# Kernel optimization log

Measured on AMD Instinct MI355X. Metric: run time of the kernel, lower is better.

Reference implementation:

```python
import jax, jax.numpy as jnp
import numpy as np

NEIGHBOUR = 3  # matches init_kwargs['neighbour']


def _conv2d(x, w, b=None, stride=1, pad=0):
    out = jax.lax.conv_general_dilated(
        x, w, (stride, stride), [(pad, pad), (pad, pad)],
        dimension_numbers=('NCHW', 'OIHW', 'NCHW'))
    if b is not None:
        out = out + b[None, :, None, None]
    return out


def _warp(x, offset, wg_w, wg_b, conv_w):
    """Deformable bilinear warp: offsets -> 4 corner gathers -> modulate -> regroup -> strided conv."""
    k = NEIGHBOUR
    N = k * k
    B, C, H, W = x.shape
    m = jax.nn.sigmoid(_conv2d(x, wg_w, wg_b, 1, 1))          # [B,N,H,W] modulation gate
    xp = jnp.pad(x, ((0, 0), (0, 0), (1, 1), (1, 1)))         # zero pad -> [B,C,H+2,W+2]
    Hp, Wp = H + 2, W + 2
    r = jnp.arange(-(k - 1) // 2, (k - 1) // 2 + 1, dtype=x.dtype)
    pnx, pny = jnp.meshgrid(r, r, indexing='ij')              # kernel-neighbour offsets p_n
    # absolute sampling positions in padded coords (p_0 starts at 1 due to padding)
    p0x = jnp.arange(1, H + 1, dtype=x.dtype)[None, :, None, None]
    p0y = jnp.arange(1, W + 1, dtype=x.dtype)[None, None, :, None]
    off = offset.transpose(0, 2, 3, 1)                        # [B,H,W,2N]; first N = x, last N = y
    px = p0x + pnx.ravel()[None, None, None, :] + off[..., :N]  # [B,H,W,N]
    py = p0y + pny.ravel()[None, None, None, :] + off[..., N:]
    fx = jnp.floor(jax.lax.stop_gradient(px))                 # p.detach().floor()
    fy = jnp.floor(jax.lax.stop_gradient(py))
    qx_lt = jnp.clip(fx, 0, Hp - 1)
    qy_lt = jnp.clip(fy, 0, Wp - 1)
    qx_rb = jnp.clip(fx + 1, 0, Hp - 1)
    qy_rb = jnp.clip(fy + 1, 0, Wp - 1)
    px = jnp.clip(px, 0, Hp - 1)
    py = jnp.clip(py, 0, Wp - 1)
    # bilinear weights (same algebra as the torch code)
    g_lt = (1 + (qx_lt - px)) * (1 + (qy_lt - py))
    g_rb = (1 - (qx_rb - px)) * (1 - (qy_rb - py))
    g_lb = (1 + (qx_lt - px)) * (1 - (qy_rb - py))
    g_rt = (1 - (qx_rb - px)) * (1 + (qy_lt - py))
    ix_lt = qx_lt.astype(jnp.int32); iy_lt = qy_lt.astype(jnp.int32)
    ix_rb = qx_rb.astype(jnp.int32); iy_rb = qy_rb.astype(jnp.int32)
    x_flat = xp.reshape(B, C, Hp * Wp)

    def gather(ix, iy):
        idx = (ix * Wp + iy).reshape(B, 1, H * W * N)
        return jnp.take_along_axis(x_flat, idx, axis=-1).reshape(B, C, H, W, N)

    xw = (g_lt[:, None] * gather(ix_lt, iy_lt)
          + g_rb[:, None] * gather(ix_rb, iy_rb)
          + g_lb[:, None] * gather(ix_lt, iy_rb)
          + g_rt[:, None] * gather(ix_rb, iy_lt))              # [B,C,H,W,N]
    xw = xw * m.transpose(0, 2, 3, 1)[:, None]                 # modulation, broadcast over C
    # regroup [B,C,H,W,k,k] -> [B,C,H*k,W*k] (matches _reshape_x_warped ordering)
    xw = xw.reshape(B, C, H, W, k, k).transpose(0, 1, 2, 4, 3, 5).reshape(B, C, H * k, W * k)
    return _conv2d(xw, conv_w, None, stride=k, pad=0)          # grouped-back strided conv


def setup_inputs() -> dict:
    B, C, MH, H, W = 4, 64, 18, 128, 128  # MH = 2*neighbour^2
    key = jax.random.key(0)
    ks = jax.random.split(key, 12)
    f32 = jnp.float32
    s = 0.05  # weight scale to keep gates unsaturated
    return {
        'x_t': jax.random.normal(ks[0], (B, C, H, W), f32),
        'pre_offset': jax.random.normal(ks[1], (B, MH, H, W), f32),
        'mean': jax.random.normal(ks[2], (B, MH, H, W), f32),
        'upd_w': s * jax.random.normal(ks[3], (MH, C + MH, 3, 3), f32),
        'upd_b': s * jax.random.normal(ks[4], (MH,), f32),
        'rst_w': s * jax.random.normal(ks[5], (MH, C + MH, 3, 3), f32),
        'rst_b': s * jax.random.normal(ks[6], (MH,), f32),
        'out_w': s * jax.random.normal(ks[7], (MH, C + MH, 3, 3), f32),
        'out_b': s * jax.random.normal(ks[8], (MH,), f32),
        'wg_w': s * jax.random.normal(ks[9], (9, C, 3, 3), f32),
        'wg_b': s * jax.random.normal(ks[10], (9,), f32),
        'warp_conv_w': s * jax.random.normal(ks[11], (C, C, 3, 3), f32),
    }


def reference(x_t, pre_offset, mean, upd_w, upd_b, rst_w, rst_b, out_w, out_b,
              wg_w, wg_b, warp_conv_w):
    stacked = jnp.concatenate([x_t, pre_offset], axis=1)
    update_gate = jax.nn.sigmoid(_conv2d(stacked, upd_w, upd_b, 1, 1))
    reset_gate = jax.nn.sigmoid(_conv2d(stacked, rst_w, rst_b, 1, 1))
    cand = jnp.tanh(_conv2d(jnp.concatenate([x_t, pre_offset * reset_gate], axis=1), out_w, out_b, 1, 1))
    offset = pre_offset * (1 - update_gate) + cand * update_gate
    mean_new = mean + 0.5 * (pre_offset - mean)
    offset = offset + mean_new
    x_out = _warp(x_t, offset, wg_w, wg_b, warp_conv_w)
    return (x_out, offset, mean_new)
```

## Files before the change

kernel.cpp:

```cpp
#include <hip/hip_runtime.h>
#include <hip/hip_bf16.h>
#include <math.h>

#define Bn  4
#define Cc  64
#define MHc 18
#define Hh  128
#define Wd  128
#define HW  (Hh*Wd)
#define Np  9
#define HP  130
#define WP  130
#define XPE (HP*WP*Cc)
#define PPE (HP*WP*32)
#define KX  576
#define KP  288
#define KT  (KX+KP)

typedef __attribute__((ext_vector_type(8))) short short8;
typedef __attribute__((ext_vector_type(4))) float float4v;

__device__ __forceinline__ float bf2f(__hip_bfloat16 x) { return __bfloat162float(x); }
__device__ __forceinline__ __hip_bfloat16 f2bf(float x) { return __float2bfloat16(x); }
__device__ __forceinline__ float sigm(float x) { return 1.f / (1.f + expf(-x)); }

#define NW1 (64*KT)
#define NW2 (32*KP)
#define NW3 (Cc*Cc*Np)

__global__ __launch_bounds__(256)
void k_prep(const float* __restrict__ x, const float* __restrict__ po,
            const float* __restrict__ upd_w, const float* __restrict__ rst_w,
            const float* __restrict__ out_w, const float* __restrict__ wg_w,
            const float* __restrict__ wcw,
            __hip_bfloat16* __restrict__ xp, __hip_bfloat16* __restrict__ pp,
            __hip_bfloat16* __restrict__ wall, __hip_bfloat16* __restrict__ w2,
            __hip_bfloat16* __restrict__ wt) {
  __shared__ float tile[16][65];
  int blk = blockIdx.x;
  int t = threadIdx.x;
  if (blk < 4096) {
    int wtile = blk & 7;
    int h = (blk >> 3) & 127;
    int b = blk >> 10;
    int w0 = wtile * 16;
    int wa = t & 15, cq = t >> 4;
    #pragma unroll
    for (int j = 0; j < 4; ++j) {
      int c = cq * 4 + j;
      tile[wa][c] = x[(b*Cc + c)*HW + h*Wd + w0 + wa];
    }
    __syncthreads();
    int cb = t & 63, wq = t >> 6;
    #pragma unroll
    for (int j = 0; j < 4; ++j) {
      int w = wq * 4 + j;
      xp[b*XPE + ((h+1)*WP + (w0 + w + 1))*Cc + cb] = f2bf(tile[w][cb]);
    }
  } else if (blk < 4608) {
    int pb = blk - 4096;
    int h = pb & 127;
    int b = pb >> 7;
    int w = t & 127;
    int half = t >> 7;
    for (int j = 0; j < 9; ++j) {
      int ch = half * 9 + j;
      float v = po[(b*MHc + ch)*HW + h*Wd + w];
      pp[b*PPE + ((h+1)*WP + (w+1))*32 + ch] = f2bf(v);
    }
  } else {
    int idx = (blk - 4608) * 256 + t;
    if (idx < NW1) {
      int k  = idx % KT;
      int gr = idx / KT;
      float v = 0.f;
      if (k < KX) {
        int n = k >> 6, ci = k & 63;
        if      (gr < 18) v = upd_w[(gr*(Cc+MHc) + ci)*9 + n];
        else if (gr < 36) v = rst_w[((gr-18)*(Cc+MHc) + ci)*9 + n];
        else if (gr < 54) v = out_w[((gr-36)*(Cc+MHc) + ci)*9 + n];
        else if (gr < 63) v = wg_w[((gr-54)*Cc + ci)*9 + n];
      } else {
        int kk = k - KX;
        int n = kk >> 5, jc = kk & 31;
        if (jc < 18) {
          if      (gr < 18) v = upd_w[(gr*(Cc+MHc) + Cc + jc)*9 + n];
          else if (gr < 36) v = rst_w[((gr-18)*(Cc+MHc) + Cc + jc)*9 + n];
        }
      }
      wall[idx] = f2bf(v);
    } else if (idx < NW1 + NW2) {
      int i2 = idx - NW1;
      int k  = i2 % KP;
      int oc = i2 / KP;
      int n = k >> 5, jc = k & 31;
      float v = (oc < 18 && jc < 18) ? out_w[(oc*(Cc+MHc) + Cc + jc)*9 + n] : 0.f;
      w2[i2] = f2bf(v);
    } else if (idx < NW1 + NW2 + NW3) {
      int i3 = idx - NW1 - NW2;
      int k  = i3 % 576;
      int co = i3 / 576;
      wt[i3] = f2bf(wcw[(co*Cc + (k & 63))*9 + (k >> 6)]);
    }
  }
}

__global__ __launch_bounds__(256)
void k_gates(const __hip_bfloat16* __restrict__ xpad,
             const __hip_bfloat16* __restrict__ popad,
             const __hip_bfloat16* __restrict__ wall,
             const float* __restrict__ po,
             const float* __restrict__ upd_b,
             const float* __restrict__ rst_b,
             const float* __restrict__ out_b,
             const float* __restrict__ wg_b,
             float* __restrict__ u_out,
             float* __restrict__ cx_out,
             __hip_bfloat16* __restrict__ ropad,
             __hip_bfloat16* __restrict__ m_t) {
  __shared__ __align__(16) __hip_bfloat16 sh[16][KT + 8];
  __shared__ __align__(16) __hip_bfloat16 roL[16][32];
  int blk = blockIdx.x;
  int wtile = blk & 7;
  int h = (blk >> 3) & 127;
  int b = blk >> 10;
  int w0 = wtile * 16;
  int lane = threadIdx.x & 63;
  int wave = threadIdx.x >> 6;
  int t = threadIdx.x;

  ((unsigned int*)roL)[t] = 0u;

  const __hip_bfloat16* xpb = xpad + b * XPE;
  const __hip_bfloat16* ppb = popad + b * PPE;
  int c32 = lane & 31, tsel = lane >> 5;

  for (int tt = 0; tt < 4; ++tt) {
    int pl = wave * 4 + tt;
    int wp = w0 + pl;
    #pragma unroll
    for (int n = 0; n < 9; ++n)
      sh[pl][n*64 + lane] = xpb[((h + n/3)*WP + wp + n%3)*Cc + lane];
    #pragma unroll
    for (int nb = 0; nb < 9; nb += 2) {
      int n = nb + tsel;
      if (n < 9)
        sh[pl][KX + n*32 + c32] = ppb[((h + n/3)*WP + wp + n%3)*32 + c32];
    }
  }
  __syncthreads();

  int mrow = lane & 15;
  int quad = lane >> 4;
  int cotile = wave * 16;
  float4v acc = {0.f, 0.f, 0.f, 0.f};
  for (int ks = 0; ks < KT/32; ++ks) {
    short8 a = *reinterpret_cast<const short8*>(
        wall + (cotile + mrow) * KT + ks * 32 + quad * 8);
    short8 bfr = *reinterpret_cast<const short8*>(
        &sh[mrow][ks * 32 + quad * 8]);
    acc = __builtin_amdgcn_mfma_f32_16x16x32_bf16(a, bfr, acc, 0, 0, 0);
  }

  int sp = h * Wd + w0 + mrow;
  #pragma unroll
  for (int r = 0; r < 4; ++r) {
    int gr = cotile + quad * 4 + r;
    float v = acc[r];
    if (gr < 18) {
      u_out[(b*MHc + gr)*HW + sp] = sigm(v + upd_b[gr]);
    } else if (gr < 36) {
      int oc = gr - 18;
      float rr = sigm(v + rst_b[oc]);
      roL[mrow][oc] = f2bf(rr * po[(b*MHc + oc)*HW + sp]);
    } else if (gr < 54) {
      int oc = gr - 36;
      cx_out[(b*MHc + oc)*HW + sp] = v + out_b[oc];
    } else if (gr < 63) {
      int nn = gr - 54;
      m_t[(b*HW + sp)*9 + nn] = f2bf(sigm(v + wg_b[nn]));
    }
  }
  __syncthreads();
  unsigned int* dst = (unsigned int*)(ropad + b*PPE + ((h+1)*WP + (w0+1))*32);
  dst[t] = ((unsigned int*)roL)[t];
}

__global__ __launch_bounds__(256)
void k_fuse(const __hip_bfloat16* __restrict__ xpad,
            const __hip_bfloat16* __restrict__ ropad,
            const __hip_bfloat16* __restrict__ w2,
            const __hip_bfloat16* __restrict__ wt,
            const __hip_bfloat16* __restrict__ m_t,
            const float* __restrict__ po,
            const float* __restrict__ mean,
            float* __restrict__ out_off,
            float* __restrict__ out_mn,
            float* __restrict__ out_x) {
  __shared__ __align__(16) char lbuf[16*584*2];
  __shared__ float offL[16][18];
  __shared__ float mL[16][9];
  __shared__ __align__(16) float gw[144][4];
  __shared__ __align__(16) int   ga[144][4];
  auto shro = (__hip_bfloat16(*)[KP+8])lbuf;
  auto xw   = (__hip_bfloat16(*)[584])lbuf;

  int blk = blockIdx.x;
  int wtile = blk & 7;
  int h = (blk >> 3) & 127;
  int b = blk >> 10;
  int w0 = wtile * 16;
  int lane = threadIdx.x & 63;
  int wave = threadIdx.x >> 6;
  int t = threadIdx.x;

  const __hip_bfloat16* rpb = ropad + b * PPE;
  int c32 = lane & 31, tsel = lane >> 5;
  for (int tt = 0; tt < 4; ++tt) {
    int pl = wave * 4 + tt;
    int wp = w0 + pl;
    #pragma unroll
    for (int nb = 0; nb < 9; nb += 2) {
      int n = nb + tsel;
      if (n < 9)
        shro[pl][n*32 + c32] = rpb[((h + n/3)*WP + wp + n%3)*32 + c32];
    }
  }
  __syncthreads();

  int mrow = lane & 15;
  int quad = lane >> 4;

  if (wave < 2) {
    float4v acc = {0.f, 0.f, 0.f, 0.f};
    for (int ks = 0; ks < KP/32; ++ks) {
      short8 a = *reinterpret_cast<const short8*>(
          w2 + (wave*16 + mrow) * KP + ks * 32 + quad * 8);
      short8 bfr = *reinterpret_cast<const short8*>(
          &shro[mrow][ks * 32 + quad * 8]);
      acc = __builtin_amdgcn_mfma_f32_16x16x32_bf16(a, bfr, acc, 0, 0, 0);
    }
    int sp = h * Wd + w0 + mrow;
    #pragma unroll
    for (int r = 0; r < 4; ++r) {
      int gr = wave*16 + quad * 4 + r;
      if (gr < 18) {
        int gi = (b*MHc + gr)*HW + sp;
        float cand = tanhf(out_off[gi] + acc[r]);
        float u = out_mn[gi];
        float p = po[gi];
        float mn = 0.5f * (mean[gi] + p);
        float off = p * (1.f - u) + cand * u + mn;
        out_off[gi] = off;
        out_mn[gi]  = mn;
        offL[mrow][gr] = off;
      }
    }
  } else {
    int base = (wave - 2) * 64 + lane;
    #pragma unroll
    for (int rep = 0; rep < 2; ++rep) {
      int id = base + rep * 128;
      if (id < 144) {
        int px = id / 9, n = id % 9;
        mL[px][n] = bf2f(m_t[(b*HW + h*Wd + w0 + px)*9 + n]);
      }
    }
  }
  __syncthreads();

  if (t < 144) {
    int px = t / 9, n = t % 9;
    int wp = w0 + px;
    float ox = offL[px][n];
    float oy = offL[px][9 + n];
    float mn = mL[px][n];
    float px_ = (float)(h + 1) + (float)(n / 3 - 1) + ox;
    float py_ = (float)(wp + 1) + (float)(n % 3 - 1) + oy;
    float fx = floorf(px_), fy = floorf(py_);
    float xlt = fminf(fmaxf(fx,       0.f), 129.f);
    float ylt = fminf(fmaxf(fy,       0.f), 129.f);
    float xrb = fminf(fmaxf(fx + 1.f, 0.f), 129.f);
    float yrb = fminf(fmaxf(fy + 1.f, 0.f), 129.f);
    float pxc = fminf(fmaxf(px_, 0.f), 129.f);
    float pyc = fminf(fmaxf(py_, 0.f), 129.f);
    float glt = (1.f + xlt - pxc) * (1.f + ylt - pyc);
    float grb = (1.f - xrb + pxc) * (1.f - yrb + pyc);
    float glb = (1.f + xlt - pxc) * (1.f - yrb + pyc);
    float grt = (1.f - xrb + pxc) * (1.f + ylt - pyc);
    int ixl = (int)xlt, iyl = (int)ylt, ixr = (int)xrb, iyr = (int)yrb;
    gw[t][0] = glt * mn; gw[t][1] = grb * mn;
    gw[t][2] = glb * mn; gw[t][3] = grt * mn;
    ga[t][0] = (ixl * WP + iyl) * Cc; ga[t][1] = (ixr * WP + iyr) * Cc;
    ga[t][2] = (ixl * WP + iyr) * Cc; ga[t][3] = (ixr * WP + iyl) * Cc;
  }
  __syncthreads();

  const __hip_bfloat16* xpb = xpad + b * XPE;
  for (int tt = 0; tt < 4; ++tt) {
    int pl = wave * 4 + tt;
    #pragma unroll
    for (int n = 0; n < Np; ++n) {
      int q = pl * 9 + n;
      float4v g = *reinterpret_cast<const float4v*>(gw[q]);
      int a0 = ga[q][0], a1 = ga[q][1], a2 = ga[q][2], a3 = ga[q][3];
      float v0 = bf2f(xpb[a0 + lane]);
      float v1 = bf2f(xpb[a1 + lane]);
      float v2 = bf2f(xpb[a2 + lane]);
      float v3 = bf2f(xpb[a3 + lane]);
      xw[pl][n * 64 + lane] = f2bf(g.x*v0 + g.y*v1 + g.z*v2 + g.w*v3);
    }
  }
  __syncthreads();

  int cotile = wave * 16;
  float4v acc = {0.f, 0.f, 0.f, 0.f};
  for (int ks = 0; ks < 18; ++ks) {
    short8 a = *reinterpret_cast<const short8*>(
        wt + (cotile + mrow) * 576 + ks * 32 + quad * 8);
    short8 bfr = *reinterpret_cast<const short8*>(
        &xw[mrow][ks * 32 + quad * 8]);
    acc = __builtin_amdgcn_mfma_f32_16x16x32_bf16(a, bfr, acc, 0, 0, 0);
  }
  #pragma unroll
  for (int r = 0; r < 4; ++r) {
    int co = cotile + quad * 4 + r;
    out_x[((b * Cc + co) * Hh + h) * Wd + w0 + mrow] = acc[r];
  }
}

__global__ void f_convAB(const float* __restrict__ x, const float* __restrict__ po,
                         const float* __restrict__ wA, const float* __restrict__ bA,
                         const float* __restrict__ wB, const float* __restrict__ bB,
                         float* __restrict__ u_scr, float* __restrict__ ro_scr) {
  int idx = blockIdx.x * 256 + threadIdx.x;
  if (idx >= Bn * MHc * HW) return;
  int w = idx & 127, h = (idx >> 7) & 127, oc = (idx >> 14) % MHc, b = idx / (MHc*HW);
  float accA = bA[oc], accB = bB[oc];
  const float* xb = x + b*Cc*HW; const float* pb = po + b*MHc*HW;
  for (int ic = 0; ic < Cc + MHc; ++ic) {
    const float* src = (ic < Cc) ? (xb + ic*HW) : (pb + (ic-Cc)*HW);
    const float* wa = wA + (oc*(Cc+MHc)+ic)*9; const float* wb = wB + (oc*(Cc+MHc)+ic)*9;
    for (int kh = 0; kh < 3; ++kh) { int hh = h+kh-1; if ((unsigned)hh >= Hh) continue;
      for (int kw = 0; kw < 3; ++kw) { int ww = w+kw-1; if ((unsigned)ww >= Wd) continue;
        float v = src[hh*Wd+ww]; accA += v*wa[kh*3+kw]; accB += v*wb[kh*3+kw]; } }
  }
  u_scr[idx] = sigm(accA); ro_scr[idx] = sigm(accB) * pb[oc*HW + h*Wd + w];
}
__global__ void f_convC(const float* __restrict__ x, const float* __restrict__ po,
                        const float* __restrict__ mean, const float* __restrict__ wC,
                        const float* __restrict__ bC, const float* __restrict__ u_scr,
                        const float* __restrict__ ro_scr, float* __restrict__ out_off,
                        float* __restrict__ out_mean) {
  int idx = blockIdx.x * 256 + threadIdx.x;
  if (idx >= Bn * MHc * HW) return;
  int w = idx & 127, h = (idx >> 7) & 127, oc = (idx >> 14) % MHc, b = idx / (MHc*HW);
  float acc = bC[oc];
  const float* xb = x + b*Cc*HW; const float* rb = ro_scr + b*MHc*HW;
  for (int ic = 0; ic < Cc + MHc; ++ic) {
    const float* src = (ic < Cc) ? (xb + ic*HW) : (rb + (ic-Cc)*HW);
    const float* wv = wC + (oc*(Cc+MHc)+ic)*9;
    for (int kh = 0; kh < 3; ++kh) { int hh = h+kh-1; if ((unsigned)hh >= Hh) continue;
      for (int kw = 0; kw < 3; ++kw) { int ww = w+kw-1; if ((unsigned)ww >= Wd) continue;
        acc += src[hh*Wd+ww]*wv[kh*3+kw]; } }
  }
  float cand = tanhf(acc); float u = u_scr[idx]; float p = po[idx];
  float mn = 0.5f*(mean[idx]+p);
  out_off[idx] = p*(1.f-u)+cand*u+mn; out_mean[idx] = mn;
}
__global__ __launch_bounds__(256)
void f_warp(const float* __restrict__ x, const float* __restrict__ off_f,
            const float* __restrict__ wg, const float* __restrict__ bg,
            const float* __restrict__ wc, float* __restrict__ out) {
  __shared__ float mred[4][Np][64]; __shared__ float mval[4][Np];
  __shared__ float xwv[4][Np][64];
  int lane = threadIdx.x & 63, wave = threadIdx.x >> 6;
  int p = blockIdx.x * 4 + wave;
  int b = p >> 14, rem = p & 16383, h = rem >> 7, w = rem & 127;
  const float* xc = x + (b*Cc + lane)*HW;
  float part[Np];
  for (int n = 0; n < Np; ++n) part[n] = 0.f;
  for (int kh = 0; kh < 3; ++kh) { int hh = h+kh-1; if ((unsigned)hh >= Hh) continue;
    for (int kw = 0; kw < 3; ++kw) { int ww = w+kw-1; if ((unsigned)ww >= Wd) continue;
      float v = xc[hh*Wd+ww];
      for (int n = 0; n < Np; ++n) part[n] += v*wg[(n*Cc+lane)*9+kh*3+kw]; } }
  for (int n = 0; n < Np; ++n) mred[wave][n][lane] = part[n];
  __syncthreads();
  if (lane < Np) { float s = bg[lane];
    for (int c = 0; c < Cc; ++c) s += mred[wave][lane][c];
    mval[wave][lane] = sigm(s); }
  __syncthreads();
  const float* offb = off_f + b*MHc*HW; int sp = h*Wd + w;
  for (int n = 0; n < Np; ++n) {
    float px = (float)(h+1) + (float)(n/3-1) + offb[n*HW+sp];
    float py = (float)(w+1) + (float)(n%3-1) + offb[(9+n)*HW+sp];
    float fxq = floorf(px), fyq = floorf(py);
    float xlt = fminf(fmaxf(fxq,0.f),129.f), ylt = fminf(fmaxf(fyq,0.f),129.f);
    float xrb = fminf(fmaxf(fxq+1.f,0.f),129.f), yrb = fminf(fmaxf(fyq+1.f,0.f),129.f);
    float pxc = fminf(fmaxf(px,0.f),129.f), pyc = fminf(fmaxf(py,0.f),129.f);
    float glt = (1.f+xlt-pxc)*(1.f+ylt-pyc), grb = (1.f-xrb+pxc)*(1.f-yrb+pyc);
    float glb = (1.f+xlt-pxc)*(1.f-yrb+pyc), grt = (1.f-xrb+pxc)*(1.f+ylt-pyc);
    int ixl=(int)xlt, iyl=(int)ylt, ixr=(int)xrb, iyr=(int)yrb;
    float vlt=0.f,vrb=0.f,vlb=0.f,vrt=0.f;
    if (ixl>=1&&ixl<=Hh&&iyl>=1&&iyl<=Wd) vlt = xc[(ixl-1)*Wd+(iyl-1)];
    if (ixr>=1&&ixr<=Hh&&iyr>=1&&iyr<=Wd) vrb = xc[(ixr-1)*Wd+(iyr-1)];
    if (ixl>=1&&ixl<=Hh&&iyr>=1&&iyr<=Wd) vlb = xc[(ixl-1)*Wd+(iyr-1)];
    if (ixr>=1&&ixr<=Hh&&iyl>=1&&iyl<=Wd) vrt = xc[(ixr-1)*Wd+(iyl-1)];
    xwv[wave][n][lane] = (glt*vlt+grb*vrb+glb*vlb+grt*vrt)*mval[wave][n];
  }
  __syncthreads();
  float acc = 0.f;
  for (int c = 0; c < Cc; ++c)
    for (int n = 0; n < Np; ++n)
      acc += xwv[wave][n][c]*wc[(lane*Cc+c)*9+n];
  out[(b*Cc+lane)*HW + h*Wd + w] = acc;
}

extern "C" void kernel_launch(void* const* d_in, const int* in_sizes, int n_in,
                              void* d_out, int out_size, void* d_ws, size_t ws_size,
                              hipStream_t stream) {
  (void)in_sizes; (void)n_in; (void)out_size;
  const float* x_t   = (const float*)d_in[0];
  const float* po    = (const float*)d_in[1];
  const float* mean  = (const float*)d_in[2];
  const float* upd_w = (const float*)d_in[3];
  const float* upd_b = (const float*)d_in[4];
  const float* rst_w = (const float*)d_in[5];
  const float* rst_b = (const float*)d_in[6];
  const float* out_w = (const float*)d_in[7];
  const float* out_b = (const float*)d_in[8];
  const float* wg_w  = (const float*)d_in[9];
  const float* wg_b  = (const float*)d_in[10];
  const float* wcw   = (const float*)d_in[11];

  float* out_x   = (float*)d_out;
  float* out_off = out_x + 4194304;
  float* out_mn  = out_off + 1179648;

  char* ws = (char*)d_ws;
  __hip_bfloat16* xpad  = (__hip_bfloat16*)(ws + 0);
  __hip_bfloat16* popad = (__hip_bfloat16*)(ws + 8652800);
  __hip_bfloat16* ropad = (__hip_bfloat16*)(ws + 12979200);
  __hip_bfloat16* wall  = (__hip_bfloat16*)(ws + 17305600);
  __hip_bfloat16* w2    = (__hip_bfloat16*)(ws + 17416192);
  __hip_bfloat16* wt_bf = (__hip_bfloat16*)(ws + 17434624);
  __hip_bfloat16* m_t   = (__hip_bfloat16*)(ws + 17508352);
  const size_t WS_NEED = 18688000;

  if (ws_size >= WS_NEED) {
    hipMemsetAsync(d_ws, 0, 17305600, stream);
    hipLaunchKernelGGL(k_prep,  dim3(5004), dim3(256), 0, stream,
                       x_t, po, upd_w, rst_w, out_w, wg_w, wcw,
                       xpad, popad, wall, w2, wt_bf);
    hipLaunchKernelGGL(k_gates, dim3(4096), dim3(256), 0, stream,
                       xpad, popad, wall, po, upd_b, rst_b, out_b, wg_b,
                       out_mn, out_off, ropad, m_t);
    hipLaunchKernelGGL(k_fuse,  dim3(4096), dim3(256), 0, stream,
                       xpad, ropad, w2, wt_bf, m_t, po, mean,
                       out_off, out_mn, out_x);
  } else {
    float* u_scr  = out_x;
    float* cx_scr = out_x + 1179648;
    hipLaunchKernelGGL(f_convAB, dim3(4608), dim3(256), 0, stream,
                       x_t, po, upd_w, upd_b, rst_w, rst_b, u_scr, cx_scr);
    hipLaunchKernelGGL(f_convC,  dim3(4608), dim3(256), 0, stream,
                       x_t, po, mean, out_w, out_b, u_scr, cx_scr,
                       out_off, out_mn);
    hipLaunchKernelGGL(f_warp,   dim3(16384), dim3(256), 0, stream,
                       x_t, out_off, wg_w, wg_b, wcw, out_x);
  }
}
```

Measured before the change: 217.5 us.

## Vectorize window staging with swizzled LDS and pair adjacent bilinear corners

k_gates and k_fuse now stage one contiguous 3-row halo window with 16-byte loads into an XOR-swizzled LDS buffer. The MFMA B-fragments index into that window directly, so the 3x3 neighbourhood is no longer duplicated per pixel and LDS bank conflicts should drop. The deformable gather now reads each pair of horizontally adjacent corners as two consecutive 128-byte rows with 16-byte vector loads, folding clipped cases into merged weights. This removes scalar 2-byte gathers, but the read past a clipped right edge can touch data beyond the row or buffer end, relying on a zero weight to cancel it.

```diff
diff --git a/kernel.cpp b/kernel.cpp
--- a/kernel.cpp
+++ b/kernel.cpp
@@ -23,6 +23,13 @@
 __device__ __forceinline__ float bf2f(__hip_bfloat16 x) { return __bfloat162float(x); }
 __device__ __forceinline__ __hip_bfloat16 f2bf(float x) { return __float2bfloat16(x); }
 __device__ __forceinline__ float sigm(float x) { return 1.f / (1.f + expf(-x)); }
+__device__ __forceinline__ float s2f(short s) {
+  return __uint_as_float(((unsigned)(unsigned short)s) << 16);
+}
+__device__ __forceinline__ short f2bs(float x) {
+  __hip_bfloat16 h = __float2bfloat16(x);
+  return *reinterpret_cast<short*>(&h);
+}
 
 #define NW1 (64*KT)
 #define NW2 (32*KP)
@@ -118,7 +125,8 @@
              float* __restrict__ cx_out,
              __hip_bfloat16* __restrict__ ropad,
              __hip_bfloat16* __restrict__ m_t) {
-  __shared__ __align__(16) __hip_bfloat16 sh[16][KT + 8];
+  __shared__ __align__(16) char winx[6912];
+  __shared__ __align__(16) char winp[3456];
   __shared__ __align__(16) __hip_bfloat16 roL[16][32];
   int blk = blockIdx.x;
   int wtile = blk & 7;
@@ -133,20 +141,20 @@
 
   const __hip_bfloat16* xpb = xpad + b * XPE;
   const __hip_bfloat16* ppb = popad + b * PPE;
-  int c32 = lane & 31, tsel = lane >> 5;
-
-  for (int tt = 0; tt < 4; ++tt) {
-    int pl = wave * 4 + tt;
-    int wp = w0 + pl;
-    #pragma unroll
-    for (int n = 0; n < 9; ++n)
-      sh[pl][n*64 + lane] = xpb[((h + n/3)*WP + wp + n%3)*Cc + lane];
-    #pragma unroll
-    for (int nb = 0; nb < 9; nb += 2) {
-      int n = nb + tsel;
-      if (n < 9)
-        sh[pl][KX + n*32 + c32] = ppb[((h + n/3)*WP + wp + n%3)*32 + c32];
-    }
+
+  for (int i = t; i < 432; i += 256) {
+    int r = i / 144, cidx = i - r * 144;
+    short8 v = *reinterpret_cast<const short8*>(
+        xpb + ((h + r) * WP + w0) * Cc + cidx * 8);
+    int o = i * 16;
+    *reinterpret_cast<short8*>(winx + (o ^ (((o >> 7) & 7) << 4))) = v;
+  }
+  if (t < 216) {
+    int r = t / 72, cidx = t - r * 72;
+    short8 v = *reinterpret_cast<const short8*>(
+        ppb + ((h + r) * WP + w0) * 32 + cidx * 8);
+    int o = t * 16;
+    *reinterpret_cast<short8*>(winp + (o ^ (((o >> 6) & 3) << 4))) = v;
   }
   __syncthreads();
 
@@ -154,11 +162,22 @@
   int quad = lane >> 4;
   int cotile = wave * 16;
   float4v acc = {0.f, 0.f, 0.f, 0.f};
+  #pragma unroll
   for (int ks = 0; ks < KT/32; ++ks) {
     short8 a = *reinterpret_cast<const short8*>(
         wall + (cotile + mrow) * KT + ks * 32 + quad * 8);
-    short8 bfr = *reinterpret_cast<const short8*>(
-        &sh[mrow][ks * 32 + quad * 8]);
+    short8 bfr;
+    if (ks < 18) {
+      int n = ks >> 1;
+      int rowidx = (n / 3) * 18 + mrow + (n % 3);
+      int lin = rowidx * 128 + (ks & 1) * 64 + quad * 16;
+      bfr = *reinterpret_cast<const short8*>(winx + (lin ^ ((rowidx & 7) << 4)));
+    } else {
+      int n = ks - 18;
+      int rowidx = (n / 3) * 18 + mrow + (n % 3);
+      int lin = rowidx * 64 + quad * 16;
+      bfr = *reinterpret_cast<const short8*>(winp + (lin ^ ((rowidx & 3) << 4)));
+    }
     acc = __builtin_amdgcn_mfma_f32_16x16x32_bf16(a, bfr, acc, 0, 0, 0);
   }
 
@@ -201,9 +220,8 @@
   __shared__ float offL[16][18];
   __shared__ float mL[16][9];
   __shared__ __align__(16) float gw[144][4];
-  __shared__ __align__(16) int   ga[144][4];
-  auto shro = (__hip_bfloat16(*)[KP+8])lbuf;
-  auto xw   = (__hip_bfloat16(*)[584])lbuf;
+  __shared__ __align__(16) int   gb[144][2];
+  auto xw = (__hip_bfloat16(*)[584])lbuf;
 
   int blk = blockIdx.x;
   int wtile = blk & 7;
@@ -215,16 +233,12 @@
   int t = threadIdx.x;
 
   const __hip_bfloat16* rpb = ropad + b * PPE;
-  int c32 = lane & 31, tsel = lane >> 5;
-  for (int tt = 0; tt < 4; ++tt) {
-    int pl = wave * 4 + tt;
-    int wp = w0 + pl;
-    #pragma unroll
-    for (int nb = 0; nb < 9; nb += 2) {
-      int n = nb + tsel;
-      if (n < 9)
-        shro[pl][n*32 + c32] = rpb[((h + n/3)*WP + wp + n%3)*32 + c32];
-    }
+  if (t < 216) {
+    int r = t / 72, cidx = t - r * 72;
+    short8 v = *reinterpret_cast<const short8*>(
+        rpb + ((h + r) * WP + w0) * 32 + cidx * 8);
+    int o = t * 16;
+    *reinterpret_cast<short8*>(lbuf + (o ^ (((o >> 6) & 3) << 4))) = v;
   }
   __syncthreads();
 
@@ -233,11 +247,14 @@
 
   if (wave < 2) {
     float4v acc = {0.f, 0.f, 0.f, 0.f};
+    #pragma unroll
     for (int ks = 0; ks < KP/32; ++ks) {
       short8 a = *reinterpret_cast<const short8*>(
           w2 + (wave*16 + mrow) * KP + ks * 32 + quad * 8);
+      int rowidx = (ks / 3) * 18 + mrow + (ks % 3);
+      int lin = rowidx * 64 + quad * 16;
       short8 bfr = *reinterpret_cast<const short8*>(
-          &shro[mrow][ks * 32 + quad * 8]);
+          lbuf + (lin ^ ((rowidx & 3) << 4)));
       acc = __builtin_amdgcn_mfma_f32_16x16x32_bf16(a, bfr, acc, 0, 0, 0);
     }
     int sp = h * Wd + w0 + mrow;
@@ -270,11 +287,12 @@
   __syncthreads();
 
   if (t < 144) {
-    int px = t / 9, n = t % 9;
+    int px = t / 9;
+    int n = t - px * 9;
     int wp = w0 + px;
     float ox = offL[px][n];
     float oy = offL[px][9 + n];
-    float mn = mL[px][n];
+    float mnv = mL[px][n];
     float px_ = (float)(h + 1) + (float)(n / 3 - 1) + ox;
     float py_ = (float)(wp + 1) + (float)(n % 3 - 1) + oy;
     float fx = floorf(px_), fy = floorf(py_);
@@ -289,27 +307,38 @@
     float glb = (1.f + xlt - pxc) * (1.f - yrb + pyc);
     float grt = (1.f - xrb + pxc) * (1.f + ylt - pyc);
     int ixl = (int)xlt, iyl = (int)ylt, ixr = (int)xrb, iyr = (int)yrb;
-    gw[t][0] = glt * mn; gw[t][1] = grb * mn;
-    gw[t][2] = glb * mn; gw[t][3] = grt * mn;
-    ga[t][0] = (ixl * WP + iyl) * Cc; ga[t][1] = (ixr * WP + iyr) * Cc;
-    ga[t][2] = (ixl * WP + iyr) * Cc; ga[t][3] = (ixr * WP + iyl) * Cc;
+    bool yAdj = (iyr == iyl + 1);
+    gw[t][0] = (glt + (yAdj ? 0.f : glb)) * mnv;
+    gw[t][1] = (yAdj ? glb : 0.f) * mnv;
+    gw[t][2] = (grt + (yAdj ? 0.f : grb)) * mnv;
+    gw[t][3] = (yAdj ? grb : 0.f) * mnv;
+    gb[t][0] = (ixl * WP + iyl) * Cc;
+    gb[t][1] = (ixr * WP + iyl) * Cc;
   }
   __syncthreads();
 
   const __hip_bfloat16* xpb = xpad + b * XPE;
-  for (int tt = 0; tt < 4; ++tt) {
-    int pl = wave * 4 + tt;
+  for (int it = t; it < 1152; it += 256) {
+    int q  = it >> 3;
+    int c0 = (it & 7) * 8;
+    float4v g = *reinterpret_cast<const float4v*>(gw[q]);
+    int bL = gb[q][0], bR = gb[q][1];
+    short8 l0 = *reinterpret_cast<const short8*>(xpb + bL + c0);
+    short8 l1 = *reinterpret_cast<const short8*>(xpb + bL + 64 + c0);
+    short8 r0 = *reinterpret_cast<const short8*>(xpb + bR + c0);
+    short8 r1 = *reinterpret_cast<const short8*>(xpb + bR + 64 + c0);
+    short8 ov;
     #pragma unroll
-    for (int n = 0; n < Np; ++n) {
-      int q = pl * 9 + n;
-      float4v g = *reinterpret_cast<const float4v*>(gw[q]);
-      int a0 = ga[q][0], a1 = ga[q][1], a2 = ga[q][2], a3 = ga[q][3];
-      float v0 = bf2f(xpb[a0 + lane]);
-      float v1 = bf2f(xpb[a1 + lane]);
-      float v2 = bf2f(xpb[a2 + lane]);
-      float v3 = bf2f(xpb[a3 + lane]);
-      xw[pl][n * 64 + lane] = f2bf(g.x*v0 + g.y*v1 + g.z*v2 + g.w*v3);
-    }
+    for (int j = 0; j < 8; ++j) {
+      float vv = g.x * s2f(l0[j]);
+      vv = fmaf(g.y, s2f(l1[j]), vv);
+      vv = fmaf(g.z, s2f(r0[j]), vv);
+      vv = fmaf(g.w, s2f(r1[j]), vv);
+      ov[j] = f2bs(vv);
+    }
+    int pl = q / 9;
+    int n  = q - pl * 9;
+    *reinterpret_cast<short8*>(&xw[pl][n * 64 + c0]) = ov;
   }
   __syncthreads();
 
```

Result: faster. 203.1 us (-6.6%).
